# Kernel optimization log

Hardware: AMD Instinct MI355X
Metric: run time of the kernel (lower is better)

The kernel has to match this reference:

```python
import jax, jax.numpy as jnp
import numpy as np

B, CIN, COUT, N, TIN = 8, 64, 64, 207, 54
K, NHID, SL, KT = 8, 64, 3, 3
HEADS, STRIDE, PL = 8, 4, 8
TIME_NUM, OUT_LEN = 120, 48
E = COUT * PL            # 512 = attention embed dim (embed_size*patch_len)
PD = E // HEADS          # 64 per-head dim
PNUM = (OUT_LEN + STRIDE - PL) // STRIDE + 1   # 12 patches
EPS = 1e-5


def setup_inputs():
    keys = iter(jax.random.split(jax.random.key(0), 48))
    def rn(shape, s):
        return jax.random.normal(next(keys), shape, jnp.float32) * s
    d = {}
    d['x'] = rn((B, CIN, N, TIN), 1.0)
    d['adj'] = jax.random.uniform(next(keys), (SL, N, N), jnp.float32) / N
    d['W_conv1'] = rn((COUT, CIN), 0.125); d['b_conv1'] = rn((COUT,), 0.02)
    d['g_T'] = jnp.ones((TIN,), jnp.float32); d['b_T'] = jnp.zeros((TIN,), jnp.float32)
    d['g_S'] = jnp.ones((N,), jnp.float32); d['b_S'] = jnp.zeros((N,), jnp.float32)
    d['W_time'] = rn((2*COUT, 3*COUT, 1, KT), 1.0/np.sqrt(3*COUT*KT)); d['b_time'] = rn((2*COUT,), 0.02)
    d['wq1'] = rn((SL, K, COUT, NHID), 0.125); d['wv1'] = rn((SL, K, COUT, NHID), 0.125)
    d['bias1'] = rn((SL, NHID), 0.05)
    d['wq2'] = rn((SL, K, NHID, 2*COUT), 0.125); d['wv2'] = rn((SL, K, NHID, 2*COUT), 0.125)
    d['bias2'] = rn((SL, 2*COUT), 0.05)
    d['W_mlp'] = rn((2*COUT, SL*2*COUT, 1, KT), 1.0/np.sqrt(SL*2*COUT*KT)); d['b_mlp'] = rn((2*COUT,), 0.02)
    d['emb_T'] = rn((TIME_NUM, E), 0.02)
    d['Wq'] = rn((PD, PD), 0.125); d['bq'] = rn((PD,), 0.02)
    d['Wk'] = rn((PD, PD), 0.125); d['bk'] = rn((PD,), 0.02)
    d['Wv'] = rn((PD, PD), 0.125); d['bv'] = rn((PD,), 0.02)
    d['W_fc'] = rn((E, E), 1.0/np.sqrt(E)); d['b_fc'] = rn((E,), 0.02)
    d['g1'] = jnp.ones((E,), jnp.float32); d['b1n'] = jnp.zeros((E,), jnp.float32)
    d['g2'] = jnp.ones((E,), jnp.float32); d['b2n'] = jnp.zeros((E,), jnp.float32)
    d['W_ff1'] = rn((E, 4*COUT), 1.0/np.sqrt(E)); d['b_ff1'] = rn((4*COUT,), 0.02)
    d['W_ff2'] = rn((4*COUT, E), 1.0/np.sqrt(4*COUT)); d['b_ff2'] = rn((E,), 0.02)
    d['W_rp'] = rn((PNUM*PL, OUT_LEN), 1.0/np.sqrt(PNUM*PL)); d['b_rp'] = rn((OUT_LEN,), 0.02)
    d['g_bn'] = jnp.ones((COUT,), jnp.float32); d['b_bn'] = jnp.zeros((COUT,), jnp.float32)
    return d


def _ln(v, g, b, axis):
    m = jnp.mean(v, axis=axis, keepdims=True)
    var = jnp.var(v, axis=axis, keepdims=True)
    xhat = (v - m) * jax.lax.rsqrt(var + EPS)
    shp = [1] * v.ndim; shp[axis] = -1
    return xhat * g.reshape(shp) + b.reshape(shp)


def _gconv(x, wq, wv, bias, a):
    # x: [B,C,N,L]; wq/wv: [K,C,D]; a: [N,N]  -- multi-basis sigmoid-gated GCN
    q = jnp.einsum('bcnl,kcd->kbdnl', x, wq)
    v = jnp.einsum('bcnl,kcd->kbdnl', x, wv)
    s = jnp.sum(jax.nn.sigmoid(q) * v, axis=0)           # [B,D,N,L]
    out = jnp.einsum('nk,bcnl->bckl', a, s)              # adjacency aggregation (exact index order of source)
    return out + bias[None, :, None, None]


def _conv2d(x, w, b, dil):
    y = jax.lax.conv_general_dilated(x, w, (1, 1), 'VALID', rhs_dilation=(1, dil),
                                     dimension_numbers=('NCHW', 'OIHW', 'NCHW'))
    return y + b[None, :, None, None]


def reference(x, adj, W_conv1, b_conv1, g_T, b_T, g_S, b_S, W_time, b_time,
              wq1, wv1, bias1, wq2, wv2, bias2, W_mlp, b_mlp, emb_T,
              Wq, bq, Wk, bk, Wv, bv, W_fc, b_fc, g1, b1n, g2, b2n,
              W_ff1, b_ff1, W_ff2, b_ff2, W_rp, b_rp, g_bn, b_bn):
    residual = jnp.einsum('oc,bcnl->bonl', W_conv1, x) + b_conv1[None, :, None, None]
    xcat = jnp.concatenate([residual, _ln(residual, g_T, b_T, 3), _ln(residual, g_S, b_S, 2)], axis=1)
    h = _conv2d(xcat, W_time, b_time, 2)                 # [B,2C,N,50]
    h = jnp.tanh(h[:, :COUT]) * jax.nn.sigmoid(h[:, COUT:])
    outs = [_gconv(jax.nn.relu(_gconv(h, wq1[i], wv1[i], bias1[i], adj[i])),
                   wq2[i], wv2[i], bias2[i], adj[i]) for i in range(SL)]
    g = _conv2d(jnp.concatenate(outs, axis=1), W_mlp, b_mlp, 1)   # [B,2C,N,48]
    g = jnp.tanh(g[:, :COUT]) * jax.nn.sigmoid(g[:, COUT:])      # [B,C,N,48]
    # --- TTransformer with patching ---
    z = jnp.pad(g, ((0, 0), (0, 0), (0, 0), (0, STRIDE)))        # pad time by stride (52 >= patch_len)
    idx = jnp.arange(PNUM)[:, None] * STRIDE + jnp.arange(PL)[None, :]
    patches = z[..., idx]                                        # [B,C,N,P,PL] unfold
    q0 = patches.reshape(B, N, PNUM, E)                          # row-major reshape, as in torch source
    xe = q0 + emb_T[:PNUM][None, None]
    qh = xe.reshape(B, N, PNUM, HEADS, PD)
    qs = qh @ Wq + bq; ks = qh @ Wk + bk; vs = qh @ Wv + bv
    scores = jnp.einsum('bnqhd,bnkhd->bnqkh', qs, ks)
    att = jax.nn.softmax(scores / jnp.sqrt(jnp.float32(E)), axis=2)   # softmax over QUERY axis (faithful to source)
    ao = jnp.einsum('bnqkh,bnkhd->bnqhd', att, vs).reshape(B, N, PNUM, E) @ W_fc + b_fc
    M = _ln(ao + xe, g1, b1n, 3)
    ff = jax.nn.relu(M @ W_ff1 + b_ff1) @ W_ff2 + b_ff2
    U = _ln(M + ff, g2, b2n, 3)
    o = (U + xe + M).reshape(B, N, COUT, PNUM * PL) @ W_rp + b_rp     # [B,N,C,48]
    o = jnp.transpose(o, (0, 2, 1, 3))                               # [B,C,N,48]
    # --- BatchNorm2d (training-mode batch stats) over residual sum ---
    y = o + residual[..., -OUT_LEN:]
    m = jnp.mean(y, axis=(0, 2, 3), keepdims=True)
    var = jnp.var(y, axis=(0, 2, 3), keepdims=True)
    return (y - m) * jax.lax.rsqrt(var + EPS) * g_bn[None, :, None, None] + b_bn[None, :, None, None]
```

## Files before the change

kernel.cpp:

```cpp
#include <hip/hip_runtime.h>
#include <hip/hip_bf16.h>

#define TPB 256
#define TPA 512

constexpr int Bx = 8, Cc = 64, Nn = 207, Tin = 54, Kb = 8;
constexpr int LP = 52, NP = Nn * LP;
constexpr int NPa = 10816;
constexpr int L50 = 50, Tout = 48;
constexpr int Ee = 512, Pn = 12;
constexpr float EPSF = 1e-5f;
constexpr int SRDF = 516;

constexpr size_t O_RESID = 0;
constexpr size_t O_LNTM  = O_RESID + (size_t)Bx*Cc*Nn*Tin;
constexpr size_t O_LNTR  = O_LNTM  + (size_t)Bx*Cc*Nn;
constexpr size_t O_LNSM  = O_LNTR  + (size_t)Bx*Cc*Nn;
constexpr size_t O_LNSR  = O_LNSM  + (size_t)Bx*Cc*Tin;
constexpr size_t O_XCAT  = O_LNSR  + (size_t)Bx*Cc*Tin;
constexpr size_t O_RB    = O_XCAT  + (size_t)Bx*192*Nn*Tin;
constexpr size_t O_H     = O_RB    + (size_t)Bx*128*NP;
constexpr size_t O_GACC  = O_H     + (size_t)Bx*64*NP;
constexpr size_t O_GG    = O_GACC  + (size_t)Bx*128*Nn*Tout;
constexpr size_t O_XE    = O_GG    + (size_t)Bx*64*Nn*Tout;
constexpr size_t O_WTT   = O_XE    + (size_t)Bx*Nn*Pn*Ee;
constexpr size_t O_WTM   = O_WTT   + (size_t)128*192*3;
constexpr size_t O_BNST  = O_WTM   + (size_t)128*384*3;
constexpr size_t O_WTB   = O_BNST + 128;
constexpr size_t O_ADJT  = O_WTB  + (size_t)128*576/2;
constexpr size_t O_HT    = O_H;
constexpr size_t O_TAIL  = O_XCAT + (size_t)Bx*128*NP;
constexpr size_t O_WQ1B  = O_TAIL + (size_t)Bx*NPa*64/2;
constexpr size_t O_WV1B  = O_WQ1B + (size_t)24*64*64/2;
constexpr size_t O_WQ2B  = O_WV1B + (size_t)24*64*64/2;
constexpr size_t O_WV2B  = O_WQ2B + (size_t)24*128*64/2;
constexpr size_t O_RBT   = O_WV2B + (size_t)24*128*64/2;
constexpr size_t O_WQT   = O_RBT  + (size_t)Bx*NPa*64/2;
constexpr size_t O_WKT   = O_WQT  + 2048;
constexpr size_t O_WVT   = O_WKT  + 2048;
constexpr size_t O_WFCT  = O_WVT  + 2048;
constexpr size_t O_WF1T  = O_WFCT + 131072;
constexpr size_t O_WF2T  = O_WF1T + 65536;

#define FMA4(acc, sA_, vB_) { (acc).x += (sA_)*(vB_).x; (acc).y += (sA_)*(vB_).y; (acc).z += (sA_)*(vB_).z; (acc).w += (sA_)*(vB_).w; }

typedef __attribute__((ext_vector_type(8))) short bf16x8;
typedef __attribute__((ext_vector_type(4))) float f32x4;

__device__ __forceinline__ float sigm(float x){ return 1.0f/(1.0f+__expf(-x)); }
__device__ __forceinline__ ushort f2bf(float x){ __hip_bfloat16 h = __float2bfloat16(x); return *(ushort*)&h; }

__global__ __launch_bounds__(TPB) void k_residual(const float* __restrict__ x, const float* __restrict__ W,
                                                  const float* __restrict__ bias, float* __restrict__ out,
                                                  float* __restrict__ lnm, float* __restrict__ lnr){
  int n = blockIdx.x, b = blockIdx.y;
  __shared__ __align__(16) float sX[Cc][Tin];
  __shared__ __align__(16) float sW[Cc*Cc];
  __shared__ __align__(16) float sO[Cc][Tin];
  int tid = threadIdx.x;
  for(int i=tid;i<Cc*Tin;i+=TPB){ int c=i/Tin, l=i%Tin; sX[c][l] = x[((size_t)(b*Cc+c)*Nn+n)*Tin+l]; }
  for(int i=tid;i<Cc*Cc;i+=TPB) sW[i]=W[i];
  __syncthreads();
  for(int i=tid;i<Cc*Tin;i+=TPB){
    int o=i/Tin, l=i%Tin; float acc=bias[o];
    #pragma unroll 8
    for(int c=0;c<Cc;c++) acc += sW[o*Cc+c]*sX[c][l];
    out[((size_t)(b*Cc+o)*Nn+n)*Tin+l]=acc;
    sO[o][l]=acc;
  }
  __syncthreads();
  if(tid < Cc){
    float s=0.f,s2=0.f;
    for(int l=0;l<Tin;l++){ float v=sO[tid][l]; s+=v; s2+=v*v; }
    float m=s*(1.f/Tin); float var=s2*(1.f/Tin)-m*m;
    int row = (b*Cc+tid)*Nn + n;
    lnm[row]=m; lnr[row]=rsqrtf(fmaxf(var,0.f)+EPSF);
  }
}

__global__ __launch_bounds__(TPB) void k_lnS(const float* __restrict__ r, float* __restrict__ mean, float* __restrict__ rstd){
  int row = blockIdx.x*TPB + threadIdx.x;
  if(row >= Bx*Cc*Tin) return;
  int l = row % Tin; int bc = row / Tin;
  const float* p = r + (size_t)bc*Nn*Tin + l;
  float s=0.f,s2=0.f;
  for(int n=0;n<Nn;n++){ float v=p[(size_t)n*Tin]; s+=v; s2+=v*v; }
  float m=s*(1.f/Nn); float var=s2*(1.f/Nn)-m*m;
  mean[row]=m; rstd[row]=rsqrtf(fmaxf(var,0.f)+EPSF);
}

struct WJob { const float* W; ushort* F; int K, N, KS, NT, sStride, total; };
struct WJobs { WJob j[11]; };

__global__ __launch_bounds__(TPB) void k_wfrag_all(WJobs jobs){
  int gi = blockIdx.x*TPB + threadIdx.x;
  for(int seg=0; seg<11; seg++){
    const WJob J = jobs.j[seg];
    if(gi < J.total){
      int i = gi;
      int j = i & 7; int lane = (i>>3) & 63;
      int t = i >> 9;
      int ks = t % J.KS; int r = t / J.KS; int colTile = r % J.NT; int s = r / J.NT;
      int r15 = lane & 15, hi = lane >> 4;
      int k = ks*32 + hi*8 + j, col = colTile*16 + r15;
      float v = (k < J.K && col < J.N) ? J.W[(size_t)s*J.sStride + (size_t)k*J.N + col] : 0.f;
      J.F[i] = f2bf(v);
      return;
    }
    gi -= J.total;
  }
}

__global__ __launch_bounds__(TPB) void k_wtbF(const float* __restrict__ W, ushort* __restrict__ F){
  int i = blockIdx.x*TPB + threadIdx.x;
  if(i >= 8*18*512) return;
  int j = i & 7; int lane = (i>>3) & 63;
  int t = i >> 9;
  int ks = t % 18; int colTile = t / 18;
  int r15 = lane & 15, hi = lane >> 4;
  int k = ks*32 + hi*8 + j, o = colTile*16 + r15;
  int kt = k/192, ci = k - kt*192;
  F[i] = f2bf(W[(size_t)(o*192+ci)*3 + kt]);
}

__global__ __launch_bounds__(TPB) void k_wmlpF(const float* __restrict__ W, ushort* __restrict__ F){
  int i = blockIdx.x*TPB + threadIdx.x;
  if(i >= 3*8*12*512) return;
  int j = i & 7; int lane = (i>>3) & 63;
  int t = i >> 9;
  int ks = t % 12; int r = t / 12; int colTile = r & 7; int layer = r >> 3;
  int r15 = lane & 15, hi = lane >> 4;
  int k = ks*32 + hi*8 + j;
  int kt = k >> 7, ci = k & 127;
  int o = colTile*16 + r15;
  F[i] = f2bf(W[(size_t)(o*384 + layer*128 + ci)*3 + kt]);
}

__global__ __launch_bounds__(TPB) void k_timeconv_mfma(const float* __restrict__ resid,
    const float* __restrict__ tm, const float* __restrict__ tr,
    const float* __restrict__ sm, const float* __restrict__ sr,
    const float* __restrict__ gT, const float* __restrict__ bT,
    const float* __restrict__ gS, const float* __restrict__ bS,
    const ushort* __restrict__ WF, const float* __restrict__ bias, ushort* __restrict__ HT){
  int n = blockIdx.x, b = blockIdx.y;
  constexpr int XS = 200;
  __shared__ __align__(16) ushort sXT[68*XS];
  int tid = threadIdx.x;
  for(int i=tid; i<14*XS; i+=TPB) sXT[54*XS + i] = 0;
  float gSn = gS[n], bSn = bS[n];
  for(int i=tid; i<64*54; i+=TPB){
    int cm = i/54, l = i%54;
    int rowT = (b*Cc+cm)*Nn + n;
    float r = resid[(size_t)rowT*Tin + l];
    float v1 = (r - tm[rowT]) * tr[rowT] * gT[l] + bT[l];
    int rowS = (b*Cc+cm)*Tin + l;
    float v2 = (r - sm[rowS]) * sr[rowS] * gSn + bSn;
    sXT[l*XS + cm]        = f2bf(r);
    sXT[l*XS + 64 + cm]   = f2bf(v1);
    sXT[l*XS + 128 + cm]  = f2bf(v2);
  }
  __syncthreads();
  int lane = tid & 63, w = tid >> 6;
  int r15 = lane & 15, hi = lane >> 4;
  float b0 = bias[w*16 + r15], b1 = bias[w*16 + 64 + r15];
  f32x4 acc0[4], acc1[4];
  #pragma unroll
  for(int tt=0;tt<4;tt++){
    acc0[tt][0]=b0; acc0[tt][1]=b0; acc0[tt][2]=b0; acc0[tt][3]=b0;
    acc1[tt][0]=b1; acc1[tt][1]=b1; acc1[tt][2]=b1; acc1[tt][3]=b1;
  }
  const ushort* wp0 = WF + ((size_t)w*18)*512 + lane*8;
  const ushort* wp1 = WF + ((size_t)(w+4)*18)*512 + lane*8;
  #pragma unroll 2
  for(int ks=0; ks<18; ks++){
    int k0 = ks*32 + hi*8;
    int kt = k0/192, ci0 = k0 - kt*192;
    bf16x8 bw0 = *(const bf16x8*)&wp0[(size_t)ks*512];
    bf16x8 bw1 = *(const bf16x8*)&wp1[(size_t)ks*512];
    #pragma unroll
    for(int tt=0;tt<4;tt++){
      bf16x8 ax = *(const bf16x8*)&sXT[(tt*16 + r15 + 2*kt)*XS + ci0];
      acc0[tt] = __builtin_amdgcn_mfma_f32_16x16x32_bf16(ax, bw0, acc0[tt], 0,0,0);
      acc1[tt] = __builtin_amdgcn_mfma_f32_16x16x32_bf16(ax, bw1, acc1[tt], 0,0,0);
    }
  }
  ushort* htp = HT + ((size_t)b*NPa + (size_t)n*LP)*64;
  int c = w*16 + r15;
  #pragma unroll
  for(int tt=0;tt<4;tt++){
    int t0 = tt*16 + hi*4;
    #pragma unroll
    for(int i=0;i<4;i++){
      int t = t0 + i;
      if(t < L50) htp[(size_t)t*64 + c] = f2bf(tanhf(acc0[tt][i])*sigm(acc1[tt][i]));
    }
  }
  if(tid < 128){ int cz = tid >> 1, tz = 50 + (tid & 1); htp[(size_t)tz*64 + cz] = 0; }
}

__global__ __launch_bounds__(TPB) void k_htpad(ushort* __restrict__ HT){
  int i = blockIdx.x*TPB + threadIdx.x;
  int per = (NPa-NP)*8;
  if(i >= Bx*per) return;
  int b = i / per, r = i % per;
  uint4 z; z.x=0;z.y=0;z.z=0;z.w=0;
  *(uint4*)&HT[((size_t)b*NPa + NP)*64 + (size_t)r*8] = z;
}

template<int D, int TR>
__global__ __launch_bounds__(TPB) void k_gcs_mfma(const ushort* __restrict__ XT,
    const ushort* __restrict__ wqF, const ushort* __restrict__ wvF,
    ushort* __restrict__ S){
  constexpr int Dt = D/16;
  int p0 = blockIdx.x*64;
  int b = blockIdx.z;
  int tid = threadIdx.x;
  int lane = tid & 63, w = tid >> 6;
  int d0 = blockIdx.y*64 + (w<<4);
  int dTile = blockIdx.y*4 + w;
  __shared__ __align__(16) ushort sX[64*64];
  if constexpr(TR){
    __shared__ __align__(16) ushort sT2[64*66];
    for(int i=tid;i<4096;i+=TPB){ int c=i>>6, col=i&63; int p=p0+col;
      sT2[c*66+col] = (p<NP) ? XT[((size_t)(b*64+c))*NP + p] : (ushort)0; }
    __syncthreads();
    for(int i=tid;i<512;i+=TPB){
      int row=i>>3, c8=(i&7)<<3;
      ushort u[8];
      #pragma unroll
      for(int j=0;j<8;j++) u[j] = sT2[(c8+j)*66 + row];
      *(uint4*)&sX[row*64 + (c8 ^ ((row&7)<<3))] = *(uint4*)u;
    }
  } else {
    for(int i=tid;i<512;i+=TPB){
      int row=i>>3, c8=(i&7)<<3;
      uint4 v = *(const uint4*)&XT[((size_t)b*NPa + p0 + row)*64 + c8];
      *(uint4*)&sX[row*64 + (c8 ^ ((row&7)<<3))] = v;
    }
  }
  __syncthreads();
  int r15 = lane & 15, hi = lane >> 4;
  bf16x8 bf[4][2];
  #pragma unroll
  for(int pt=0;pt<4;pt++){
    int row = pt*16 + r15;
    int sw = (row&7)<<3;
    int cu0 = hi*8;
    bf[pt][0] = *(const bf16x8*)&sX[row*64 + (cu0 ^ sw)];
    bf[pt][1] = *(const bf16x8*)&sX[row*64 + ((cu0+32) ^ sw)];
  }
  f32x4 acc[4];
  #pragma unroll
  for(int pt=0;pt<4;pt++){ acc[pt][0]=0.f; acc[pt][1]=0.f; acc[pt][2]=0.f; acc[pt][3]=0.f; }
  const ushort* wqp = wqF + ((size_t)dTile*2)*512 + lane*8;
  const ushort* wvp = wvF + ((size_t)dTile*2)*512 + lane*8;
  for(int k=0;k<Kb;k++){
    bf16x8 aq0 = *(const bf16x8*)&wqp[0];
    bf16x8 aq1 = *(const bf16x8*)&wqp[512];
    bf16x8 av0 = *(const bf16x8*)&wvp[0];
    bf16x8 av1 = *(const bf16x8*)&wvp[512];
    wqp += (size_t)Dt*2*512; wvp += (size_t)Dt*2*512;
    #pragma unroll
    for(int pt=0;pt<4;pt++){
      f32x4 q; q[0]=0.f;q[1]=0.f;q[2]=0.f;q[3]=0.f;
      f32x4 v; v[0]=0.f;v[1]=0.f;v[2]=0.f;v[3]=0.f;
      q = __builtin_amdgcn_mfma_f32_16x16x32_bf16(aq0, bf[pt][0], q, 0,0,0);
      q = __builtin_amdgcn_mfma_f32_16x16x32_bf16(aq1, bf[pt][1], q, 0,0,0);
      v = __builtin_amdgcn_mfma_f32_16x16x32_bf16(av0, bf[pt][0], v, 0,0,0);
      v = __builtin_amdgcn_mfma_f32_16x16x32_bf16(av1, bf[pt][1], v, 0,0,0);
      #pragma unroll
      for(int i=0;i<4;i++) acc[pt][i] += v[i]*sigm(q[i]);
    }
  }
  #pragma unroll
  for(int pt=0;pt<4;pt++){
    int p = p0 + pt*16 + r15;
    if(p < NP){
      #pragma unroll
      for(int i=0;i<4;i++){
        int d = d0 + hi*4 + i;
        S[((size_t)b*D + d)*NP + p] = f2bf(acc[pt][i]);
      }
    }
  }
}

template<int RELU>
__global__ __launch_bounds__(TPB) void k_agg_mfma(const ushort* __restrict__ S, const ushort* __restrict__ adjF,
                                                  const float* __restrict__ bias, ushort* __restrict__ Out, int D){
  int d = blockIdx.x, b = blockIdx.y;
  int bd = b*D + d;
  constexpr int SST = 232;
  __shared__ __align__(16) ushort sB[64*SST];
  int tid = threadIdx.x;
  for(int i=tid*8; i<64*SST; i+=TPB*8){ uint4 z; z.x=0;z.y=0;z.z=0;z.w=0; *(uint4*)&sB[i]=z; }
  __syncthreads();
  const ushort* Sp = S + (size_t)bd*NP;
  for(int i=tid; i<NP; i+=TPB){
    int nn = i/52, l = i - nn*52;
    sB[l*SST + nn] = Sp[i];
  }
  __syncthreads();
  int lane = tid & 63, w = tid >> 6;
  int r15 = lane & 15, hi = lane >> 4;
  float bb = bias[d];
  ushort* Op = Out + (size_t)bd*NP;
  for(int k2t = w; k2t < 13; k2t += 4){
    f32x4 acc[4];
    #pragma unroll
    for(int lt=0;lt<4;lt++){ acc[lt][0]=0;acc[lt][1]=0;acc[lt][2]=0;acc[lt][3]=0; }
    #pragma unroll
    for(int ks=0; ks<7; ks++){
      bf16x8 a = *(const bf16x8*)&adjF[((size_t)(k2t*7 + ks))*512 + lane*8];
      #pragma unroll
      for(int lt=0;lt<4;lt++){
        bf16x8 bfr = *(const bf16x8*)&sB[(lt*16+r15)*SST + ks*32 + hi*8];
        acc[lt] = __builtin_amdgcn_mfma_f32_16x16x32_bf16(a, bfr, acc[lt], 0,0,0);
      }
    }
    #pragma unroll
    for(int lt=0;lt<4;lt++){
      #pragma unroll
      for(int i2=0;i2<4;i2++){
        int k2 = k2t*16 + hi*4 + i2;
        int l  = lt*16 + r15;
        if(k2 < Nn && l < LP){
          float v = acc[lt][i2] + bb;
          if(RELU) v = fmaxf(v, 0.f);
          Op[(size_t)k2*LP + l] = f2bf(v);
        }
      }
    }
  }
}

template<int MODE>
__global__ __launch_bounds__(TPB) void k_mlpacc_mfma(const ushort* __restrict__ RB, const ushort* __restrict__ WF,
                                                     float* __restrict__ gacc, const float* __restrict__ bm,
                                                     float* __restrict__ gg){
  int n = blockIdx.x, b = blockIdx.y;
  constexpr int CS = 136;
  __shared__ __align__(16) ushort sLT[52*CS];
  int tid = threadIdx.x;
  for(int i=tid;i<6656;i+=TPB){
    int c = i/52, l = i%52;
    sLT[l*CS + c] = RB[(((size_t)b*128+c)*Nn + n)*LP + l];
  }
  __syncthreads();
  int lane = tid & 63, w = tid >> 6;
  int r15 = lane & 15, hi = lane >> 4;
  f32x4 acc0[3], acc1[3];
  #pragma unroll
  for(int tt=0;tt<3;tt++){
    acc0[tt][0]=0;acc0[tt][1]=0;acc0[tt][2]=0;acc0[tt][3]=0;
    acc1[tt][0]=0;acc1[tt][1]=0;acc1[tt][2]=0;acc1[tt][3]=0;
  }
  const ushort* wp0 = WF + ((size_t)w*12)*512 + lane*8;
  const ushort* wp1 = WF + ((size_t)(w+4)*12)*512 + lane*8;
  #pragma unroll 3
  for(int ks=0; ks<12; ks++){
    int kt = ks>>2, ci0 = (ks&3)*32 + hi*8;
    bf16x8 bw0 = *(const bf16x8*)&wp0[(size_t)ks*512];
    bf16x8 bw1 = *(const bf16x8*)&wp1[(size_t)ks*512];
    #pragma unroll
    for(int tt=0;tt<3;tt++){
      bf16x8 ax = *(const bf16x8*)&sLT[(tt*16 + r15 + kt)*CS + ci0];
      acc0[tt] = __builtin_amdgcn_mfma_f32_16x16x32_bf16(ax, bw0, acc0[tt], 0,0,0);
      acc1[tt] = __builtin_amdgcn_mfma_f32_16x16x32_bf16(ax, bw1, acc1[tt], 0,0,0);
    }
  }
  int o = w*16 + r15;
  if(MODE < 2){
    float* gp = gacc + ((size_t)b*Nn + n)*48*128;
    #pragma unroll
    for(int tt=0;tt<3;tt++){
      #pragma unroll
      for(int i2=0;i2<4;i2++){
        int tq = tt*16 + hi*4 + i2;
        size_t a0 = (size_t)tq*128 + o;
        if(MODE==0){ gp[a0] = acc0[tt][i2]; gp[a0+64] = acc1[tt][i2]; }
        else       { gp[a0] += acc0[tt][i2]; gp[a0+64] += acc1[tt][i2]; }
      }
    }
  } else {
    const float* gp = gacc + ((size_t)b*Nn + n)*48*128;
    float b0 = bm[o], b1 = bm[o+64];
    float* ggp = gg + (((size_t)b*Cc + o)*Nn + n)*(size_t)Tout;
    #pragma unroll
    for(int tt=0;tt<3;tt++){
      #pragma unroll
      for(int i2=0;i2<4;i2++){
        int tq = tt*16 + hi*4 + i2;
        size_t a0 = (size_t)tq*128 + o;
        float a  = gp[a0]    + acc0[tt][i2] + b0;
        float g2 = gp[a0+64] + acc1[tt][i2] + b1;
        ggp[tq] = tanhf(a)*sigm(g2);
      }
    }
  }
}

__global__ __launch_bounds__(TPB) void k_xe(const float* __restrict__ gg, const float* __restrict__ emb, float* __restrict__ xe){
  size_t i = (size_t)blockIdx.x*TPB + threadIdx.x;
  if(i >= (size_t)Bx*1271808) return;
  int b = (int)(i / 1271808);
  int off = (int)(i % 1271808);
  int c = off / 19872; int r = off % 19872;
  int n = r / 96; int r2 = r % 96;
  int p = r2 >> 3; int j = r2 & 7;
  int t = p*4 + j;
  float v = 0.f;
  if(t < Tout) v = gg[(((size_t)b*Cc+c)*Nn + n)*Tout + t];
  int e = off & 511; int p2 = (off >> 9) % 12;
  xe[i] = v + emb[(size_t)p2*Ee + e];
}

template<int NW>
__device__ __forceinline__ void ln_rows(float* buf, const float* __restrict__ g, const float* __restrict__ be, int tid){
  int lane = tid & 63, wv = tid >> 6;
  for(int r = wv; r < 12; r += NW){
    float s=0.f, s2=0.f;
    #pragma unroll
    for(int j=0;j<8;j++){ float v = buf[r*SRDF + j*64 + lane]; s+=v; s2+=v*v; }
    #pragma unroll
    for(int off=32; off; off>>=1){ s += __shfl_xor(s,off); s2 += __shfl_xor(s2,off); }
    float m = s*(1.f/512.f);
    float rstd = rsqrtf(fmaxf(s2*(1.f/512.f)-m*m, 0.f)+EPSF);
    #pragma unroll
    for(int j=0;j<8;j++){ int e = j*64+lane; float v = buf[r*SRDF+e];
      buf[r*SRDF+e] = (v-m)*rstd*g[e] + be[e]; }
  }
}

__global__ __launch_bounds__(TPA,2) void k_attn(
    const float* __restrict__ xe, const float* __restrict__ resid,
    const ushort* __restrict__ WqF, const float* __restrict__ bq,
    const ushort* __restrict__ WkF, const float* __restrict__ bk,
    const ushort* __restrict__ WvF, const float* __restrict__ bv,
    const ushort* __restrict__ WfcF, const float* __restrict__ bfc,
    const float* __restrict__ g1, const float* __restrict__ b1n,
    const float* __restrict__ g2, const float* __restrict__ b2n,
    const ushort* __restrict__ Wff1F, const float* __restrict__ bff1,
    const ushort* __restrict__ Wff2F, const float* __restrict__ bff2,
    const float* __restrict__ Wrp, const float* __restrict__ brp,
    float* __restrict__ y)
{
  int n = blockIdx.x, b = blockIdx.y;
  __shared__ __align__(16) ushort SbX[16*512];
  __shared__ __align__(16) ushort Mb[16*256];
  __shared__ __align__(16) float U0[12*SRDF];
  __shared__ __align__(16) float U1[12*SRDF];
  __shared__ __align__(16) float sS[1160];
  int tid = threadIdx.x;
  int lane = tid & 63, w = tid >> 6;
  int r15 = lane & 15, hi = lane >> 4;
  const float* __restrict__ xeg = xe + ((size_t)b*Nn + n)*6144;

  for(int i=tid;i<1024;i+=TPA){
    int r = i>>6, ch = i&63;
    ushort u[8];
    if(r<12){
      const float* s = &xeg[r*512 + ch*8];
      #pragma unroll
      for(int j=0;j<8;j++) u[j] = f2bf(s[j]);
    } else {
      #pragma unroll
      for(int j=0;j<8;j++) u[j] = 0;
    }
    *(uint4*)&SbX[r*512 + ((ch ^ (r&7))<<3)] = *(uint4*)u;
  }
  for(int i=tid;i<128;i+=TPA){
    int r = 12 + (i>>5), ch = i&31;
    uint4 z; z.x=0;z.y=0;z.z=0;z.w=0;
    *(uint4*)&Mb[r*256 + ch*8] = z;
  }
  __syncthreads();

  f32x4 vfrag[4];
  {
    int head = w;
    bf16x8 a0, a1;
    { int ch0 = head*8 + hi, ch1 = head*8 + 4 + hi;
      a0 = *(const bf16x8*)&SbX[r15*512 + ((ch0 ^ (r15&7))<<3)];
      a1 = *(const bf16x8*)&SbX[r15*512 + ((ch1 ^ (r15&7))<<3)]; }
    #pragma unroll
    for(int nt=0;nt<4;nt++){
      int col = nt*16 + r15;
      float bb = bq[col];
      f32x4 acc; acc[0]=bb;acc[1]=bb;acc[2]=bb;acc[3]=bb;
      acc = __builtin_amdgcn_mfma_f32_16x16x32_bf16(a0, *(const bf16x8*)&WqF[(size_t)(nt*2+0)*512 + lane*8], acc, 0,0,0);
      acc = __builtin_amdgcn_mfma_f32_16x16x32_bf16(a1, *(const bf16x8*)&WqF[(size_t)(nt*2+1)*512 + lane*8], acc, 0,0,0);
      #pragma unroll
      for(int i2=0;i2<4;i2++){ int p = hi*4+i2; if(p<12) U0[p*SRDF + head*64 + col] = acc[i2]; }
    }
    #pragma unroll
    for(int nt=0;nt<4;nt++){
      int col = nt*16 + r15;
      float bb = bk[col];
      f32x4 acc; acc[0]=bb;acc[1]=bb;acc[2]=bb;acc[3]=bb;
      acc = __builtin_amdgcn_mfma_f32_16x16x32_bf16(a0, *(const bf16x8*)&WkF[(size_t)(nt*2+0)*512 + lane*8], acc, 0,0,0);
      acc = __builtin_amdgcn_mfma_f32_16x16x32_bf16(a1, *(const bf16x8*)&WkF[(size_t)(nt*2+1)*512 + lane*8], acc, 0,0,0);
      #pragma unroll
      for(int i2=0;i2<4;i2++){ int p = hi*4+i2; if(p<12) U1[p*SRDF + head*64 + col] = acc[i2]; }
    }
    #pragma unroll
    for(int nt=0;nt<4;nt++){
      int col = nt*16 + r15;
      float bb = bv[col];
      f32x4 acc; acc[0]=bb;acc[1]=bb;acc[2]=bb;acc[3]=bb;
      acc = __builtin_amdgcn_mfma_f32_16x16x32_bf16(a0, *(const bf16x8*)&WvF[(size_t)(nt*2+0)*512 + lane*8], acc, 0,0,0);
      acc = __builtin_amdgcn_mfma_f32_16x16x32_bf16(a1, *(const bf16x8*)&WvF[(size_t)(nt*2+1)*512 + lane*8], acc, 0,0,0);
      vfrag[nt] = acc;
    }
  }
  __syncthreads();

  const float scale = 0.04419417382415922f;
  for(int i=tid;i<1152;i+=TPA){
    int q = i%12, kh = i/12; int h2 = kh&7, k2 = kh>>3;
    const float* qp = &U0[q*SRDF + h2*64];
    const float* kp = &U1[k2*SRDF + h2*64];
    float s=0.f;
    #pragma unroll
    for(int d4=0; d4<16; d4++){
      float4 a4 = *(const float4*)&qp[d4*4];
      float4 b4 = *(const float4*)&kp[d4*4];
      s += a4.x*b4.x + a4.y*b4.y + a4.z*b4.z + a4.w*b4.w;
    }
    sS[i] = s*scale;
  }
  __syncthreads();
  {
    int head = w;
    #pragma unroll
    for(int nt=0;nt<4;nt++){
      int col = nt*16 + r15;
      #pragma unroll
      for(int i2=0;i2<4;i2++){ int p = hi*4+i2; if(p<12) U0[p*SRDF + head*64 + col] = vfrag[nt][i2]; }
    }
  }
  if(tid<96){
    float mx=-1e30f;
    for(int q=0;q<12;q++) mx = fmaxf(mx, sS[tid*12+q]);
    float sm=0.f;
    for(int q=0;q<12;q++){ float e = __expf(sS[tid*12+q]-mx); sS[tid*12+q]=e; sm+=e; }
    float inv = 1.f/sm;
    for(int q=0;q<12;q++) sS[tid*12+q] *= inv;
  }
  __syncthreads();

  for(int i=tid;i<6144;i+=TPA){
    int q=i>>9, h2=(i>>6)&7, d=i&63;
    float s=0.f;
    #pragma unroll
    for(int k2=0;k2<12;k2++) s += sS[(k2*8+h2)*12+q]*U0[k2*SRDF+h2*64+d];
    int kk = i & 511;
    SbX[q*512 + (((kk>>3) ^ (q&7))<<3) + (kk&7)] = f2bf(s);
  }
  __syncthreads();

  {
    f32x4 acc[4];
    #pragma unroll
    for(int nt=0;nt<4;nt++){ float bb = bfc[(w*4+nt)*16 + r15]; acc[nt][0]=bb;acc[nt][1]=bb;acc[nt][2]=bb;acc[nt][3]=bb; }
    for(int ks=0;ks<16;ks++){
      int ch = ks*4 + hi;
      bf16x8 a = *(const bf16x8*)&SbX[r15*512 + ((ch ^ (r15&7))<<3)];
      #pragma unroll
      for(int nt=0;nt<4;nt++){
        acc[nt] = __builtin_amdgcn_mfma_f32_16x16x32_bf16(a, *(const bf16x8*)&WfcF[(size_t)((w*4+nt)*16 + ks)*512 + lane*8], acc[nt], 0,0,0);
      }
    }
    #pragma unroll
    for(int nt=0;nt<4;nt++){
      int col = (w*4+nt)*16 + r15;
      #pragma unroll
      for(int i2=0;i2<4;i2++){ int p = hi*4+i2; if(p<12) U1[p*SRDF + col] = acc[nt][i2] + xeg[p*512 + col]; }
    }
  }
  __syncthreads();
  ln_rows<8>(U1, g1, b1n, tid);
  __syncthreads();

  for(int i=tid;i<6144;i+=TPA){
    int r=i>>9, kk=i&511;
    SbX[r*512 + (((kk>>3) ^ (r&7))<<3) + (kk&7)] = f2bf(U1[r*SRDF + kk]);
  }
  __syncthreads();

  {
    f32x4 acc[2];
    #pragma unroll
    for(int nt=0;nt<2;nt++){ float bb = bff1[(w*2+nt)*16 + r15]; acc[nt][0]=bb;acc[nt][1]=bb;acc[nt][2]=bb;acc[nt][3]=bb; }
    for(int ks=0;ks<16;ks++){
      int ch = ks*4 + hi;
      bf16x8 a = *(const bf16x8*)&SbX[r15*512 + ((ch ^ (r15&7))<<3)];
      #pragma unroll
      for(int nt=0;nt<2;nt++){
        acc[nt] = __builtin_amdgcn_mfma_f32_16x16x32_bf16(a, *(const bf16x8*)&Wff1F[(size_t)((w*2+nt)*16 + ks)*512 + lane*8], acc[nt], 0,0,0);
      }
    }
    #pragma unroll
    for(int nt=0;nt<2;nt++){
      int u = (w*2+nt)*16 + r15;
      #pragma unroll
      for(int i2=0;i2<4;i2++){
        int p = hi*4+i2;
        if(p<12) Mb[p*256 + (((u>>3) ^ (p&7))<<3) + (u&7)] = f2bf(fmaxf(acc[nt][i2], 0.f));
      }
    }
  }
  __syncthreads();

  {
    f32x4 acc[4];
    #pragma unroll
    for(int nt=0;nt<4;nt++){ float bb = bff2[(w*4+nt)*16 + r15]; acc[nt][0]=bb;acc[nt][1]=bb;acc[nt][2]=bb;acc[nt][3]=bb; }
    for(int ks=0;ks<8;ks++){
      int ch = ks*4 + hi;
      bf16x8 a = *(const bf16x8*)&Mb[r15*256 + ((ch ^ (r15&7))<<3)];
      #pragma unroll
      for(int nt=0;nt<4;nt++){
        acc[nt] = __builtin_amdgcn_mfma_f32_16x16x32_bf16(a, *(const bf16x8*)&Wff2F[(size_t)((w*4+nt)*8 + ks)*512 + lane*8], acc[nt], 0,0,0);
      }
    }
    #pragma unroll
    for(int nt=0;nt<4;nt++){
      int col = (w*4+nt)*16 + r15;
      #pragma unroll
      for(int i2=0;i2<4;i2++){ int p = hi*4+i2; if(p<12) U0[p*SRDF + col] = acc[nt][i2] + U1[p*SRDF + col]; }
    }
  }
  __syncthreads();
  ln_rows<8>(U0, g2, b2n, tid);
  __syncthreads();

  for(int i=tid;i<6144;i+=TPA){
    int r=i>>9, c=i&511;
    U1[r*SRDF+c] = U0[r*SRDF+c] + U1[r*SRDF+c] + xeg[r*512+c];
  }
  __syncthreads();
  for(int i=tid;i<4608;i+=TPA) U0[i] = Wrp[i];
  __syncthreads();
  #pragma unroll
  for(int j=0;j<2;j++){
    int i4 = tid + j*TPA;
    if(i4 < 768){
      int c = i4/12, tq = i4%12; int t0 = tq*4;
      float4 acc = *(const float4*)&brp[t0];
      for(int t96=0;t96<96;t96++){
        int f = c*96 + t96;
        float a = U1[(f>>9)*SRDF + (f&511)];
        float4 w4 = *(const float4*)&U0[t96*48 + t0];
        FMA4(acc, a, w4);
      }
      size_t rb = (((size_t)b*Cc+c)*Nn + n)*Tin + 6 + t0;
      acc.x += resid[rb+0]; acc.y += resid[rb+1]; acc.z += resid[rb+2]; acc.w += resid[rb+3];
      *(float4*)&y[(((size_t)b*Cc+c)*Nn + n)*Tout + t0] = acc;
    }
  }
}

__global__ __launch_bounds__(TPB) void k_bnstats(const float* __restrict__ y, float* __restrict__ stats){
  int c = blockIdx.x; int tid = threadIdx.x;
  float s=0.f,s2=0.f;
  const int per = Nn*Tout;
  for(int idx=tid; idx<Bx*per; idx+=TPB){
    int b = idx/per, r = idx%per;
    float v = y[((size_t)b*Cc+c)*per + r];
    s+=v; s2+=v*v;
  }
  __shared__ float rs[TPB], rs2[TPB];
  rs[tid]=s; rs2[tid]=s2; __syncthreads();
  for(int off=TPB/2; off; off>>=1){ if(tid<off){ rs[tid]+=rs[tid+off]; rs2[tid]+=rs2[tid+off]; } __syncthreads(); }
  if(tid==0){
    float m = rs[0]/(float)(Bx*per);
    float var = rs2[0]/(float)(Bx*per) - m*m;
    stats[c]=m; stats[64+c]=rsqrtf(fmaxf(var,0.f)+EPSF);
  }
}
__global__ __launch_bounds__(TPB) void k_bnout(const float* __restrict__ y, const float* __restrict__ stats,
                                               const float* __restrict__ gbn, const float* __restrict__ bbn,
                                               float* __restrict__ out){
  size_t i = (size_t)blockIdx.x*TPB + threadIdx.x;
  if(i >= (size_t)Bx*Cc*Nn*Tout) return;
  int c = (int)((i/(Nn*Tout))%Cc);
  out[i] = (y[i]-stats[c])*stats[64+c]*gbn[c] + bbn[c];
}

extern "C" void kernel_launch(void* const* d_in, const int* in_sizes, int n_in,
                              void* d_out, int out_size, void* d_ws, size_t ws_size,
                              hipStream_t stream) {
  const float* x      = (const float*)d_in[0];
  const float* adj    = (const float*)d_in[1];
  const float* Wconv1 = (const float*)d_in[2];
  const float* bconv1 = (const float*)d_in[3];
  const float* gT     = (const float*)d_in[4];
  const float* bT     = (const float*)d_in[5];
  const float* gS     = (const float*)d_in[6];
  const float* bS     = (const float*)d_in[7];
  const float* Wtime  = (const float*)d_in[8];
  const float* btime  = (const float*)d_in[9];
  const float* wq1    = (const float*)d_in[10];
  const float* wv1    = (const float*)d_in[11];
  const float* bias1  = (const float*)d_in[12];
  const float* wq2    = (const float*)d_in[13];
  const float* wv2    = (const float*)d_in[14];
  const float* bias2  = (const float*)d_in[15];
  const float* Wmlp   = (const float*)d_in[16];
  const float* bmlp   = (const float*)d_in[17];
  const float* embT   = (const float*)d_in[18];
  const float* Wq     = (const float*)d_in[19];
  const float* bq     = (const float*)d_in[20];
  const float* Wk     = (const float*)d_in[21];
  const float* bk     = (const float*)d_in[22];
  const float* Wv     = (const float*)d_in[23];
  const float* bv     = (const float*)d_in[24];
  const float* Wfc    = (const float*)d_in[25];
  const float* bfc    = (const float*)d_in[26];
  const float* g1     = (const float*)d_in[27];
  const float* b1n    = (const float*)d_in[28];
  const float* g2     = (const float*)d_in[29];
  const float* b2n    = (const float*)d_in[30];
  const float* Wff1   = (const float*)d_in[31];
  const float* bff1   = (const float*)d_in[32];
  const float* Wff2   = (const float*)d_in[33];
  const float* bff2   = (const float*)d_in[34];
  const float* Wrp    = (const float*)d_in[35];
  const float* brp    = (const float*)d_in[36];
  const float* gbn    = (const float*)d_in[37];
  const float* bbn    = (const float*)d_in[38];

  float* ws = (float*)d_ws;
  float* RESID = ws + O_RESID;
  float* LNTM  = ws + O_LNTM;
  float* LNTR  = ws + O_LNTR;
  float* LNSM  = ws + O_LNSM;
  float* LNSR  = ws + O_LNSR;
  ushort* RA   = (ushort*)(ws + O_XCAT);
  ushort* RB   = (ushort*)(ws + O_RB);
  float* GACC  = ws + O_GACC;
  float* GG    = ws + O_GG;
  float* Y     = ws + O_GG;
  float* XE    = ws + O_XE;
  float* BNST  = ws + O_BNST;
  ushort* WTMF = (ushort*)(ws + O_WTM);
  ushort* WTB  = (ushort*)(ws + O_WTB);
  ushort* ADJT = (ushort*)(ws + O_ADJT);
  ushort* HT   = (ushort*)(ws + O_HT);
  ushort* WQ1B = (ushort*)(ws + O_WQ1B);
  ushort* WV1B = (ushort*)(ws + O_WV1B);
  ushort* WQ2B = (ushort*)(ws + O_WQ2B);
  ushort* WV2B = (ushort*)(ws + O_WV2B);
  ushort* WQT  = (ushort*)(ws + O_WQT);
  ushort* WKT  = (ushort*)(ws + O_WKT);
  ushort* WVT  = (ushort*)(ws + O_WVT);
  ushort* WFCT = (ushort*)(ws + O_WFCT);
  ushort* WF1T = (ushort*)(ws + O_WF1T);
  ushort* WF2T = (ushort*)(ws + O_WF2T);

  k_residual<<<dim3(Nn,Bx),TPB,0,stream>>>(x, Wconv1, bconv1, RESID, LNTM, LNTR);
  k_lnS<<<(Bx*Cc*Tin)/TPB,TPB,0,stream>>>(RESID, LNSM, LNSR);
  k_wtbF<<<(8*18*512+TPB-1)/TPB,TPB,0,stream>>>(Wtime, WTB);
  k_wmlpF<<<(3*8*12*512+TPB-1)/TPB,TPB,0,stream>>>(Wmlp, WTMF);
  k_htpad<<<(Bx*(NPa-NP)*8+TPB-1)/TPB,TPB,0,stream>>>(HT);
  k_timeconv_mfma<<<dim3(Nn,Bx),TPB,0,stream>>>(RESID, LNTM, LNTR, LNSM, LNSR, gT, bT, gS, bS,
                                                WTB, btime, HT);

  WJobs jobs;
  jobs.j[0]  = { wq1,  WQ1B, 64,  64,  2,  4,  64*64,   24*4*2*512 };
  jobs.j[1]  = { wv1,  WV1B, 64,  64,  2,  4,  64*64,   24*4*2*512 };
  jobs.j[2]  = { wq2,  WQ2B, 64,  128, 2,  8,  64*128,  24*8*2*512 };
  jobs.j[3]  = { wv2,  WV2B, 64,  128, 2,  8,  64*128,  24*8*2*512 };
  jobs.j[4]  = { Wq,   WQT,  64,  64,  2,  4,  64*64,   4*2*512 };
  jobs.j[5]  = { Wk,   WKT,  64,  64,  2,  4,  64*64,   4*2*512 };
  jobs.j[6]  = { Wv,   WVT,  64,  64,  2,  4,  64*64,   4*2*512 };
  jobs.j[7]  = { Wfc,  WFCT, 512, 512, 16, 32, 512*512, 32*16*512 };
  jobs.j[8]  = { Wff1, WF1T, 512, 256, 16, 16, 512*256, 16*16*512 };
  jobs.j[9]  = { Wff2, WF2T, 256, 512, 8,  32, 256*512, 32*8*512 };
  jobs.j[10] = { adj,  ADJT, 207, 207, 7,  13, Nn*Nn,   3*13*7*512 };
  int totalW = 2*(24*4*2*512) + 2*(24*8*2*512) + 3*(4*2*512) + 32*16*512 + 16*16*512 + 32*8*512 + 3*13*7*512;
  k_wfrag_all<<<(totalW+TPB-1)/TPB,TPB,0,stream>>>(jobs);

  for(int i=0;i<3;i++){
    k_gcs_mfma<64,0><<<dim3(169,1,Bx),TPB,0,stream>>>(HT, WQ1B+(size_t)i*8*4*2*512, WV1B+(size_t)i*8*4*2*512, RA);
    k_agg_mfma<1><<<dim3(64,Bx),TPB,0,stream>>>(RA, ADJT+(size_t)i*13*7*512, bias1+(size_t)i*64, RB, 64);
    k_gcs_mfma<128,1><<<dim3(169,2,Bx),TPB,0,stream>>>(RB, WQ2B+(size_t)i*8*8*2*512, WV2B+(size_t)i*8*8*2*512, RA);
    k_agg_mfma<0><<<dim3(128,Bx),TPB,0,stream>>>(RA, ADJT+(size_t)i*13*7*512, bias2+(size_t)i*128, RB, 128);
    if(i==0)      k_mlpacc_mfma<0><<<dim3(Nn,Bx),TPB,0,stream>>>(RB, WTMF+(size_t)i*8*12*512, GACC, bmlp, GG);
    else if(i==1) k_mlpacc_mfma<1><<<dim3(Nn,Bx),TPB,0,stream>>>(RB, WTMF+(size_t)i*8*12*512, GACC, bmlp, GG);
    else          k_mlpacc_mfma<2><<<dim3(Nn,Bx),TPB,0,stream>>>(RB, WTMF+(size_t)i*8*12*512, GACC, bmlp, GG);
  }
  k_xe<<<(Bx*1271808)/TPB,TPB,0,stream>>>(GG, embT, XE);
  k_attn<<<dim3(Nn,Bx),TPA,0,stream>>>(XE, RESID, WQT,bq, WKT,bk, WVT,bv, WFCT,bfc,
                                       g1,b1n,g2,b2n, WF1T,bff1, WF2T,bff2, Wrp,brp, Y);
  k_bnstats<<<64,TPB,0,stream>>>(Y, BNST);
  k_bnout<<<(Bx*Cc*Nn*Tout)/TPB,TPB,0,stream>>>(Y, BNST, gbn, bbn, (float*)d_out);
}
```

Baseline: 869.6 us.

## Fuse three per-layer MLP accumulation launches into one kernel over all layers

Each of the three graph-conv layers now keeps its output in its own workspace buffer, and a single MLP kernel stages all three into shared memory and accumulates every layer's contribution in registers. This removes the fp32 GACC read-modify-write round trips and two kernel launches. In exchange the kernel uses three times the LDS per block, which may reduce occupancy, and the workspace is reused with aliased regions (RB2 placed after RA, S1 in the old GACC space), which depends on those regions being large enough.

```diff
diff --git a/kernel.cpp b/kernel.cpp
--- a/kernel.cpp
+++ b/kernel.cpp
@@ -334,17 +334,20 @@
   }
 }
 
-template<int MODE>
-__global__ __launch_bounds__(TPB) void k_mlpacc_mfma(const ushort* __restrict__ RB, const ushort* __restrict__ WF,
-                                                     float* __restrict__ gacc, const float* __restrict__ bm,
-                                                     float* __restrict__ gg){
+__global__ __launch_bounds__(TPB) void k_mlp_all(const ushort* __restrict__ RB0, const ushort* __restrict__ RB1,
+                                                 const ushort* __restrict__ RB2, const ushort* __restrict__ WF,
+                                                 const float* __restrict__ bm, float* __restrict__ gg){
   int n = blockIdx.x, b = blockIdx.y;
   constexpr int CS = 136;
-  __shared__ __align__(16) ushort sLT[52*CS];
+  __shared__ __align__(16) ushort sLT[3*52*CS];
   int tid = threadIdx.x;
-  for(int i=tid;i<6656;i+=TPB){
-    int c = i/52, l = i%52;
-    sLT[l*CS + c] = RB[(((size_t)b*128+c)*Nn + n)*LP + l];
+  {
+    const ushort* Rp = RB0;
+    for(int i=tid;i<6656;i+=TPB){ int c=i/52, l=i%52; sLT[0*52*CS + l*CS + c] = Rp[(((size_t)b*128+c)*Nn + n)*LP + l]; }
+    Rp = RB1;
+    for(int i=tid;i<6656;i+=TPB){ int c=i/52, l=i%52; sLT[1*52*CS + l*CS + c] = Rp[(((size_t)b*128+c)*Nn + n)*LP + l]; }
+    Rp = RB2;
+    for(int i=tid;i<6656;i+=TPB){ int c=i/52, l=i%52; sLT[2*52*CS + l*CS + c] = Rp[(((size_t)b*128+c)*Nn + n)*LP + l]; }
   }
   __syncthreads();
   int lane = tid & 63, w = tid >> 6;
@@ -355,47 +358,35 @@
     acc0[tt][0]=0;acc0[tt][1]=0;acc0[tt][2]=0;acc0[tt][3]=0;
     acc1[tt][0]=0;acc1[tt][1]=0;acc1[tt][2]=0;acc1[tt][3]=0;
   }
-  const ushort* wp0 = WF + ((size_t)w*12)*512 + lane*8;
-  const ushort* wp1 = WF + ((size_t)(w+4)*12)*512 + lane*8;
-  #pragma unroll 3
-  for(int ks=0; ks<12; ks++){
-    int kt = ks>>2, ci0 = (ks&3)*32 + hi*8;
-    bf16x8 bw0 = *(const bf16x8*)&wp0[(size_t)ks*512];
-    bf16x8 bw1 = *(const bf16x8*)&wp1[(size_t)ks*512];
-    #pragma unroll
-    for(int tt=0;tt<3;tt++){
-      bf16x8 ax = *(const bf16x8*)&sLT[(tt*16 + r15 + kt)*CS + ci0];
-      acc0[tt] = __builtin_amdgcn_mfma_f32_16x16x32_bf16(ax, bw0, acc0[tt], 0,0,0);
-      acc1[tt] = __builtin_amdgcn_mfma_f32_16x16x32_bf16(ax, bw1, acc1[tt], 0,0,0);
+  #pragma unroll
+  for(int layer=0; layer<3; layer++){
+    const ushort* wp0 = WF + ((size_t)(layer*8 + w)*12)*512 + lane*8;
+    const ushort* wp1 = WF + ((size_t)(layer*8 + w+4)*12)*512 + lane*8;
+    const ushort* sL = &sLT[layer*52*CS];
+    #pragma unroll 3
+    for(int ks=0; ks<12; ks++){
+      int kt = ks>>2, ci0 = (ks&3)*32 + hi*8;
+      bf16x8 bw0 = *(const bf16x8*)&wp0[(size_t)ks*512];
+      bf16x8 bw1 = *(const bf16x8*)&wp1[(size_t)ks*512];
+      #pragma unroll
+      for(int tt=0;tt<3;tt++){
+        bf16x8 ax = *(const bf16x8*)&sL[(tt*16 + r15 + kt)*CS + ci0];
+        acc0[tt] = __builtin_amdgcn_mfma_f32_16x16x32_bf16(ax, bw0, acc0[tt], 0,0,0);
+        acc1[tt] = __builtin_amdgcn_mfma_f32_16x16x32_bf16(ax, bw1, acc1[tt], 0,0,0);
+      }
     }
   }
   int o = w*16 + r15;
-  if(MODE < 2){
-    float* gp = gacc + ((size_t)b*Nn + n)*48*128;
-    #pragma unroll
-    for(int tt=0;tt<3;tt++){
-      #pragma unroll
-      for(int i2=0;i2<4;i2++){
-        int tq = tt*16 + hi*4 + i2;
-        size_t a0 = (size_t)tq*128 + o;
-        if(MODE==0){ gp[a0] = acc0[tt][i2]; gp[a0+64] = acc1[tt][i2]; }
-        else       { gp[a0] += acc0[tt][i2]; gp[a0+64] += acc1[tt][i2]; }
-      }
-    }
-  } else {
-    const float* gp = gacc + ((size_t)b*Nn + n)*48*128;
-    float b0 = bm[o], b1 = bm[o+64];
-    float* ggp = gg + (((size_t)b*Cc + o)*Nn + n)*(size_t)Tout;
-    #pragma unroll
-    for(int tt=0;tt<3;tt++){
-      #pragma unroll
-      for(int i2=0;i2<4;i2++){
-        int tq = tt*16 + hi*4 + i2;
-        size_t a0 = (size_t)tq*128 + o;
-        float a  = gp[a0]    + acc0[tt][i2] + b0;
-        float g2 = gp[a0+64] + acc1[tt][i2] + b1;
-        ggp[tq] = tanhf(a)*sigm(g2);
-      }
+  float b0 = bm[o], b1 = bm[o+64];
+  float* ggp = gg + (((size_t)b*Cc + o)*Nn + n)*(size_t)Tout;
+  #pragma unroll
+  for(int tt=0;tt<3;tt++){
+    #pragma unroll
+    for(int i2=0;i2<4;i2++){
+      int tq = tt*16 + hi*4 + i2;
+      float a  = acc0[tt][i2] + b0;
+      float g2 = acc1[tt][i2] + b1;
+      ggp[tq] = tanhf(a)*sigm(g2);
     }
   }
 }
@@ -738,8 +729,10 @@
   float* LNSM  = ws + O_LNSM;
   float* LNSR  = ws + O_LNSR;
   ushort* RA   = (ushort*)(ws + O_XCAT);
-  ushort* RB   = (ushort*)(ws + O_RB);
-  float* GACC  = ws + O_GACC;
+  ushort* RB2  = RA + (size_t)Bx*128*NP;
+  ushort* RB0  = (ushort*)(ws + O_RB);
+  ushort* RB1  = RB0 + (size_t)Bx*128*NP;
+  ushort* S1   = (ushort*)(ws + O_GACC);
   float* GG    = ws + O_GG;
   float* Y     = ws + O_GG;
   float* XE    = ws + O_XE;
@@ -782,15 +775,14 @@
   int totalW = 2*(24*4*2*512) + 2*(24*8*2*512) + 3*(4*2*512) + 32*16*512 + 16*16*512 + 32*8*512 + 3*13*7*512;
   k_wfrag_all<<<(totalW+TPB-1)/TPB,TPB,0,stream>>>(jobs);
 
+  ushort* RBv[3] = { RB0, RB1, RB2 };
   for(int i=0;i<3;i++){
     k_gcs_mfma<64,0><<<dim3(169,1,Bx),TPB,0,stream>>>(HT, WQ1B+(size_t)i*8*4*2*512, WV1B+(size_t)i*8*4*2*512, RA);
-    k_agg_mfma<1><<<dim3(64,Bx),TPB,0,stream>>>(RA, ADJT+(size_t)i*13*7*512, bias1+(size_t)i*64, RB, 64);
-    k_gcs_mfma<128,1><<<dim3(169,2,Bx),TPB,0,stream>>>(RB, WQ2B+(size_t)i*8*8*2*512, WV2B+(size_t)i*8*8*2*512, RA);
-    k_agg_mfma<0><<<dim3(128,Bx),TPB,0,stream>>>(RA, ADJT+(size_t)i*13*7*512, bias2+(size_t)i*128, RB, 128);
-    if(i==0)      k_mlpacc_mfma<0><<<dim3(Nn,Bx),TPB,0,stream>>>(RB, WTMF+(size_t)i*8*12*512, GACC, bmlp, GG);
-    else if(i==1) k_mlpacc_mfma<1><<<dim3(Nn,Bx),TPB,0,stream>>>(RB, WTMF+(size_t)i*8*12*512, GACC, bmlp, GG);
-    else          k_mlpacc_mfma<2><<<dim3(Nn,Bx),TPB,0,stream>>>(RB, WTMF+(size_t)i*8*12*512, GACC, bmlp, GG);
-  }
+    k_agg_mfma<1><<<dim3(64,Bx),TPB,0,stream>>>(RA, ADJT+(size_t)i*13*7*512, bias1+(size_t)i*64, S1, 64);
+    k_gcs_mfma<128,1><<<dim3(169,2,Bx),TPB,0,stream>>>(S1, WQ2B+(size_t)i*8*8*2*512, WV2B+(size_t)i*8*8*2*512, RA);
+    k_agg_mfma<0><<<dim3(128,Bx),TPB,0,stream>>>(RA, ADJT+(size_t)i*13*7*512, bias2+(size_t)i*128, RBv[i], 128);
+  }
+  k_mlp_all<<<dim3(Nn,Bx),TPB,0,stream>>>(RB0, RB1, RB2, WTMF, bmlp, GG);
   k_xe<<<(Bx*1271808)/TPB,TPB,0,stream>>>(GG, embT, XE);
   k_attn<<<dim3(Nn,Bx),TPA,0,stream>>>(XE, RESID, WQT,bq, WKT,bk, WVT,bv, WFCT,bfc,
                                        g1,b1n,g2,b2n, WF1T,bff1, WF2T,bff2, Wrp,brp, Y);
```

New measurement: 858.5 us. Within noise of the previous version (-1.3%).
